# Kernel optimization log

Hardware: AMD Instinct MI355X
Metric: run time of the kernel (lower is better)

Reference implementation:

```python
import jax, jax.numpy as jnp
import numpy as np

NUM_HEADS = 8
S = 8192
D = 64          # PROJECTION_WIDTH
WORD_WIDTH = 512  # NUM_HEADS * D


def setup_inputs() -> dict:
    key = jax.random.key(0)
    kq, kk, kv, kw = jax.random.split(key, 4)
    q = jax.random.normal(kq, (S, D), dtype=jnp.float32)
    k = jax.random.normal(kk, (S, D), dtype=jnp.float32)
    v = jax.random.normal(kv, (S, D), dtype=jnp.float32)
    w_o = jax.random.normal(kw, (NUM_HEADS * D, WORD_WIDTH), dtype=jnp.float32)
    return {"q": q, "k": k, "v": v, "w_o": w_o}


def reference(q, k, v, w_o):
    # q_dot_k = q @ k.T / sqrt(d); softmax over dim=1 (rows); no mask.
    scale = 1.0 / jnp.sqrt(jnp.asarray(q.shape[1], dtype=q.dtype))
    scores = jnp.einsum('sd,td->st', q, k) * scale          # [S, S]
    attn = jax.nn.softmax(scores, axis=1)                   # [S, S]
    head = jnp.einsum('st,td->sd', attn, v)                 # [S, D]
    # All NUM_HEADS SelfAttentionLayers share the same (q,k,v) and have no
    # per-head parameters, so concatenating the heads is a tile of one head.
    concat = jnp.tile(head, (1, NUM_HEADS))                 # [S, NUM_HEADS*D]
    return concat @ w_o                                     # [S, WORD_WIDTH]
```

## Files before the change

### kernel.cpp

```cpp
#include <hip/hip_runtime.h>
#include <hip/hip_bf16.h>

typedef _Float16 half8 __attribute__((ext_vector_type(8)));
typedef __fp16 fp16x2 __attribute__((ext_vector_type(2)));
typedef __attribute__((ext_vector_type(4))) float floatx4;
typedef __attribute__((ext_vector_type(2))) float floatx2;

#define MFMAH(a, b, c) __builtin_amdgcn_mfma_f32_16x16x32_f16((a), (b), (c), 0, 0, 0)

#define SEQ 8192
#define SCALE_LOG2E 0.18033688011112042f

__device__ __forceinline__ unsigned pkh(float a, float b) {
    union { fp16x2 h; unsigned u; } cv;
    cv.h = __builtin_amdgcn_cvt_pkrtz(a, b);
    return cv.u;
}
__device__ __forceinline__ void gload16(const void* gptr, void* lptr) {
    __builtin_amdgcn_global_load_lds(
        (const __attribute__((address_space(1))) void*)gptr,
        (__attribute__((address_space(3))) void*)lptr, 16, 0, 0);
}
__device__ __forceinline__ void block_barrier() {
    asm volatile("" ::: "memory");
    __builtin_amdgcn_s_barrier();
    asm volatile("" ::: "memory");
}

__global__ __launch_bounds__(256) void prep_kernel(
        const float* __restrict__ kg, const float* __restrict__ vg,
        const float* __restrict__ w_o, _Float16* __restrict__ kf,
        _Float16* __restrict__ vt, float* __restrict__ weff) {
    const int bid = blockIdx.x, tid = threadIdx.x;
    if (bid < 256) {
        int e = (bid * 256 + tid) * 8;
        floatx4 a = *(const floatx4*)(kg + e);
        floatx4 b = *(const floatx4*)(kg + e + 4);
        half8 h;
        h[0] = (_Float16)a[0]; h[1] = (_Float16)a[1]; h[2] = (_Float16)a[2]; h[3] = (_Float16)a[3];
        h[4] = (_Float16)b[0]; h[5] = (_Float16)b[1]; h[6] = (_Float16)b[2]; h[7] = (_Float16)b[3];
        *(half8*)(kf + e) = h;
    } else if (bid < 384) {
        __shared__ _Float16 T[64][72];
        const int t0 = (bid - 256) * 64;
        {
            int r = tid >> 2, cs = (tid & 3) * 16;
            const float* vp = vg + (size_t)(t0 + r) * 64 + cs;
            half8 h0, h1;
#pragma unroll
            for (int j = 0; j < 8; ++j) { h0[j] = (_Float16)vp[j]; h1[j] = (_Float16)vp[8 + j]; }
            *(half8*)&T[r][cs] = h0;
            *(half8*)&T[r][cs + 8] = h1;
        }
        __syncthreads();
        {
            int d = tid >> 2, ts = (tid & 3) * 16;
            half8 o0, o1;
#pragma unroll
            for (int j = 0; j < 8; ++j) { o0[j] = T[ts + j][d]; o1[j] = T[ts + 8 + j][d]; }
            *(half8*)(vt + (size_t)d * SEQ + t0 + ts) = o0;
            *(half8*)(vt + (size_t)d * SEQ + t0 + ts + 8) = o1;
        }
    } else {
        int idx = (bid - 384) * 256 + tid;
        int d = idx >> 9, j = idx & 511;
        float s = 0.f;
#pragma unroll
        for (int h = 0; h < 8; ++h) s += w_o[((h * 64 + d) << 9) + j];
        weff[idx] = s;
    }
}

__global__ __launch_bounds__(256, 4) void flash_kernel(
        const float* __restrict__ qg, const _Float16* __restrict__ kf,
        const _Float16* __restrict__ vt, float* __restrict__ pacc,
        float* __restrict__ pl, int kvlen) {
    __shared__ __align__(16) char smem[32768];

    const int tid  = threadIdx.x;
    const int lane = tid & 63;
    const int w    = tid >> 6;
    const int l15  = lane & 15;
    const int kgi  = lane >> 4;
    const int qbase = blockIdx.x * 128;
    const int split = blockIdx.y;
    const int kv0   = split * kvlen;
    const int nt    = kvlen >> 6;

    const int r0 = tid >> 3;
    const int g8 = (((tid & 7) ^ (r0 & 7)) << 3);
    const int pr0 = ((r0 >> 2) & 3) * 8 + ((r0 >> 4) & 1) * 4 + (r0 & 3);

    auto STAGE = [&](int bsel, int kvb) {
        char* b = smem + bsel * 16384;
        const size_t ko = (size_t)(kvb + pr0) * 64 + g8;
        const size_t vo = (size_t)r0 * SEQ + kvb + g8;
        gload16(kf + ko,                    b + tid * 16);
        gload16(kf + ko + 32 * 64,          b + 4096  + tid * 16);
        gload16(vt + vo,                    b + 8192  + tid * 16);
        gload16(vt + vo + (size_t)32 * SEQ, b + 12288 + tid * 16);
    };

    const float* qp = qg + (size_t)(qbase + w * 32 + l15) * 64 + kgi * 8;
    floatx4 qv[2][2][2];
#pragma unroll
    for (int qf = 0; qf < 2; ++qf)
#pragma unroll
        for (int kc = 0; kc < 2; ++kc) {
            qv[qf][kc][0] = *(const floatx4*)(qp + qf * 16 * 64 + kc * 32);
            qv[qf][kc][1] = *(const floatx4*)(qp + qf * 16 * 64 + kc * 32 + 4);
        }

    STAGE(0, kv0);
    STAGE(1, kv0 + 64);

    half8 qh[2][2];
#pragma unroll
    for (int qf = 0; qf < 2; ++qf)
#pragma unroll
        for (int kc = 0; kc < 2; ++kc) {
            half8 h;
#pragma unroll
            for (int i = 0; i < 4; ++i) {
                h[i]     = (_Float16)(qv[qf][kc][0][i] * SCALE_LOG2E);
                h[i + 4] = (_Float16)(qv[qf][kc][1][i] * SCALE_LOG2E);
            }
            qh[qf][kc] = h;
        }

    floatx4 acc[2][4];
#pragma unroll
    for (int qf = 0; qf < 2; ++qf)
#pragma unroll
        for (int i = 0; i < 4; ++i) acc[qf][i] = (floatx4){0.f, 0.f, 0.f, 0.f};
    floatx4 lacc[2] = {(floatx4){0.f, 0.f, 0.f, 0.f}, (floatx4){0.f, 0.f, 0.f, 0.f}};
    const half8 vone = {(_Float16)1.f, (_Float16)1.f, (_Float16)1.f, (_Float16)1.f,
                        (_Float16)1.f, (_Float16)1.f, (_Float16)1.f, (_Float16)1.f};

    asm volatile("s_waitcnt vmcnt(4)" ::: "memory");
    block_barrier();

    for (int t = 0; t < nt; ++t) {
        const _Float16* KL = (const _Float16*)(smem + (t & 1) * 16384);
        const _Float16* VL = KL + 4096;

        floatx4 st[2][4];
#pragma unroll
        for (int qf = 0; qf < 2; ++qf)
#pragma unroll
            for (int ct = 0; ct < 4; ++ct) st[qf][ct] = (floatx4){0.f, 0.f, 0.f, 0.f};
        __builtin_amdgcn_s_setprio(1);
#pragma unroll
        for (int ct = 0; ct < 4; ++ct) {
            const int row = ct * 16 + l15;
#pragma unroll
            for (int kc = 0; kc < 2; ++kc) {
                const int go = (((kc * 4 + kgi) ^ (row & 7)) << 3);
                const half8 kh = *(const half8*)(KL + row * 64 + go);
                st[0][ct] = MFMAH(kh, qh[0][kc], st[0][ct]);
                st[1][ct] = MFMAH(kh, qh[1][kc], st[1][ct]);
            }
        }
        __builtin_amdgcn_s_setprio(0);

        half8 pbh[2][2];
#pragma unroll
        for (int qf = 0; qf < 2; ++qf) {
#pragma unroll
            for (int ct = 0; ct < 4; ++ct)
#pragma unroll
                for (int r = 0; r < 4; ++r)
                    st[qf][ct][r] = __builtin_amdgcn_exp2f(st[qf][ct][r]);
#pragma unroll
            for (int kc = 0; kc < 2; ++kc) {
                union { unsigned u[4]; half8 h; } pb;
                pb.u[0] = pkh(st[qf][2 * kc][0],     st[qf][2 * kc][1]);
                pb.u[1] = pkh(st[qf][2 * kc][2],     st[qf][2 * kc][3]);
                pb.u[2] = pkh(st[qf][2 * kc + 1][0], st[qf][2 * kc + 1][1]);
                pb.u[3] = pkh(st[qf][2 * kc + 1][2], st[qf][2 * kc + 1][3]);
                pbh[qf][kc] = pb.h;
            }
        }

        __builtin_amdgcn_s_setprio(1);
#pragma unroll
        for (int kc = 0; kc < 2; ++kc) {
            lacc[0] = MFMAH(vone, pbh[0][kc], lacc[0]);
            lacc[1] = MFMAH(vone, pbh[1][kc], lacc[1]);
#pragma unroll
            for (int db = 0; db < 4; ++db) {
                const int row = db * 16 + l15;
                const int go = (((kc * 4 + kgi) ^ (row & 7)) << 3);
                const half8 va = *(const half8*)(VL + row * 64 + go);
                acc[0][db] = MFMAH(va, pbh[0][kc], acc[0][db]);
                acc[1][db] = MFMAH(va, pbh[1][kc], acc[1][db]);
            }
        }
        __builtin_amdgcn_s_setprio(0);

        if (t + 1 < nt) {
            block_barrier();
            if (t + 2 < nt) {
                STAGE(t & 1, kv0 + (t + 2) * 64);
                asm volatile("s_waitcnt vmcnt(4)" ::: "memory");
            } else {
                asm volatile("s_waitcnt vmcnt(0)" ::: "memory");
            }
            block_barrier();
        }
    }

    block_barrier();
    float* Tw = (float*)(smem + w * 4352);
#pragma unroll
    for (int qf = 0; qf < 2; ++qf) {
#pragma unroll
        for (int db = 0; db < 4; ++db)
#pragma unroll
            for (int r = 0; r < 4; ++r)
                Tw[l15 * 68 + db * 16 + kgi * 4 + r] = acc[qf][db][r];
        {
            const int qrow = lane >> 2, gg = lane & 3;
            float* orow = pacc + ((size_t)split * SEQ + qbase + w * 32 + qf * 16 + qrow) * 64 + gg * 16;
#pragma unroll
            for (int i = 0; i < 4; ++i)
                *(floatx4*)(orow + i * 4) = *(const floatx4*)&Tw[qrow * 68 + gg * 16 + i * 4];
        }
        if (lane < 16) {
            pl[(size_t)split * SEQ + qbase + w * 32 + qf * 16 + lane] = lacc[qf][0];
        }
        __builtin_amdgcn_s_barrier();
    }
}

__global__ __launch_bounds__(256) void combineproj_kernel(
        const float* __restrict__ pacc, const float* __restrict__ pl,
        const float* __restrict__ weff, float* __restrict__ out, int KS) {
    __shared__ float hlds[16][64];
    const int tid = threadIdx.x;
    const int s0 = blockIdx.x * 16;
    {
        const int row = tid >> 4, d0 = (tid & 15) * 4;
        const int qq = s0 + row;
        floatx4 A = (floatx4){0.f, 0.f, 0.f, 0.f};
        float L = 0.f;
        for (int s2 = 0; s2 < KS; ++s2) {
            L += pl[(size_t)s2 * SEQ + qq];
            A += *(const floatx4*)&pacc[((size_t)s2 * SEQ + qq) * 64 + d0];
        }
        A *= (1.0f / L);
        *(floatx4*)&hlds[row][d0] = A;
    }
    __syncthreads();
    const int j0 = tid * 2;
    float a0[16], a1[16];
#pragma unroll
    for (int s = 0; s < 16; ++s) { a0[s] = 0.f; a1[s] = 0.f; }
    for (int d4 = 0; d4 < 16; ++d4) {
        floatx2 wv[4];
#pragma unroll
        for (int dd = 0; dd < 4; ++dd)
            wv[dd] = *(const floatx2*)&weff[(size_t)(d4 * 4 + dd) * 512 + j0];
#pragma unroll
        for (int s = 0; s < 16; ++s) {
            floatx4 h = *(const floatx4*)&hlds[s][d4 * 4];
#pragma unroll
            for (int dd = 0; dd < 4; ++dd) {
                a0[s] += h[dd] * wv[dd][0];
                a1[s] += h[dd] * wv[dd][1];
            }
        }
    }
#pragma unroll
    for (int s = 0; s < 16; ++s) {
        floatx2 o = {a0[s], a1[s]};
        *(floatx2*)&out[(size_t)(s0 + s) * 512 + j0] = o;
    }
}

extern "C" void kernel_launch(void* const* d_in, const int* in_sizes, int n_in,
                              void* d_out, int out_size, void* d_ws, size_t ws_size,
                              hipStream_t stream) {
    const float* q   = (const float*)d_in[0];
    const float* k   = (const float*)d_in[1];
    const float* v   = (const float*)d_in[2];
    const float* w_o = (const float*)d_in[3];
    float* out = (float*)d_out;

    const size_t weff_sz = 64 * 512 * sizeof(float);
    const size_t h_sz    = (size_t)SEQ * 64 * sizeof(_Float16);
    auto need = [&](int ks) {
        return weff_sz + 2 * h_sz
               + (size_t)ks * SEQ * 64 * sizeof(float)
               + (size_t)ks * SEQ * sizeof(float);
    };
    int KS = 1;
    if (ws_size >= need(8)) KS = 8;
    else if (ws_size >= need(4)) KS = 4;
    else if (ws_size >= need(2)) KS = 2;

    char* p = (char*)d_ws;
    float* weff = (float*)p;  p += weff_sz;
    float* pacc = (float*)p;  p += (size_t)KS * SEQ * 64 * sizeof(float);
    float* pl   = (float*)p;  p += (size_t)KS * SEQ * sizeof(float);
    _Float16* kf = (_Float16*)p;  p += h_sz;
    _Float16* vt = (_Float16*)p;

    prep_kernel<<<dim3(512), dim3(256), 0, stream>>>(k, v, w_o, kf, vt, weff);
    flash_kernel<<<dim3(SEQ / 128, KS), dim3(256), 0, stream>>>(q, kf, vt, pacc, pl, SEQ / KS);
    combineproj_kernel<<<dim3(SEQ / 16), dim3(256), 0, stream>>>(pacc, pl, weff, out, KS);
}
```

Baseline: 107.6 us.

## Double query rows per flash block and add a 16-way KV split

```diff
diff --git a/kernel.cpp b/kernel.cpp
--- a/kernel.cpp
+++ b/kernel.cpp
@@ -71,7 +71,7 @@
     }
 }
 
-__global__ __launch_bounds__(256, 4) void flash_kernel(
+__global__ __launch_bounds__(256, 2) void flash_kernel(
         const float* __restrict__ qg, const _Float16* __restrict__ kf,
         const _Float16* __restrict__ vt, float* __restrict__ pacc,
         float* __restrict__ pl, int kvlen) {
@@ -82,7 +82,7 @@
     const int w    = tid >> 6;
     const int l15  = lane & 15;
     const int kgi  = lane >> 4;
-    const int qbase = blockIdx.x * 128;
+    const int qbase = blockIdx.x * 256;
     const int split = blockIdx.y;
     const int kv0   = split * kvlen;
     const int nt    = kvlen >> 6;
@@ -101,10 +101,10 @@
         gload16(vt + vo + (size_t)32 * SEQ, b + 12288 + tid * 16);
     };
 
-    const float* qp = qg + (size_t)(qbase + w * 32 + l15) * 64 + kgi * 8;
-    floatx4 qv[2][2][2];
-#pragma unroll
-    for (int qf = 0; qf < 2; ++qf)
+    const float* qp = qg + (size_t)(qbase + w * 64 + l15) * 64 + kgi * 8;
+    floatx4 qv[4][2][2];
+#pragma unroll
+    for (int qf = 0; qf < 4; ++qf)
 #pragma unroll
         for (int kc = 0; kc < 2; ++kc) {
             qv[qf][kc][0] = *(const floatx4*)(qp + qf * 16 * 64 + kc * 32);
@@ -114,9 +114,9 @@
     STAGE(0, kv0);
     STAGE(1, kv0 + 64);
 
-    half8 qh[2][2];
-#pragma unroll
-    for (int qf = 0; qf < 2; ++qf)
+    half8 qh[4][2];
+#pragma unroll
+    for (int qf = 0; qf < 4; ++qf)
 #pragma unroll
         for (int kc = 0; kc < 2; ++kc) {
             half8 h;
@@ -128,12 +128,14 @@
             qh[qf][kc] = h;
         }
 
-    floatx4 acc[2][4];
-#pragma unroll
-    for (int qf = 0; qf < 2; ++qf)
+    floatx4 acc[4][4];
+#pragma unroll
+    for (int qf = 0; qf < 4; ++qf)
 #pragma unroll
         for (int i = 0; i < 4; ++i) acc[qf][i] = (floatx4){0.f, 0.f, 0.f, 0.f};
-    floatx4 lacc[2] = {(floatx4){0.f, 0.f, 0.f, 0.f}, (floatx4){0.f, 0.f, 0.f, 0.f}};
+    floatx4 lacc[4];
+#pragma unroll
+    for (int qf = 0; qf < 4; ++qf) lacc[qf] = (floatx4){0.f, 0.f, 0.f, 0.f};
     const half8 vone = {(_Float16)1.f, (_Float16)1.f, (_Float16)1.f, (_Float16)1.f,
                         (_Float16)1.f, (_Float16)1.f, (_Float16)1.f, (_Float16)1.f};
 
@@ -144,40 +146,42 @@
         const _Float16* KL = (const _Float16*)(smem + (t & 1) * 16384);
         const _Float16* VL = KL + 4096;
 
-        floatx4 st[2][4];
-#pragma unroll
-        for (int qf = 0; qf < 2; ++qf)
-#pragma unroll
-            for (int ct = 0; ct < 4; ++ct) st[qf][ct] = (floatx4){0.f, 0.f, 0.f, 0.f};
-        __builtin_amdgcn_s_setprio(1);
+        half8 khr[4][2];
 #pragma unroll
         for (int ct = 0; ct < 4; ++ct) {
             const int row = ct * 16 + l15;
 #pragma unroll
             for (int kc = 0; kc < 2; ++kc) {
                 const int go = (((kc * 4 + kgi) ^ (row & 7)) << 3);
-                const half8 kh = *(const half8*)(KL + row * 64 + go);
-                st[0][ct] = MFMAH(kh, qh[0][kc], st[0][ct]);
-                st[1][ct] = MFMAH(kh, qh[1][kc], st[1][ct]);
-            }
-        }
-        __builtin_amdgcn_s_setprio(0);
-
-        half8 pbh[2][2];
-#pragma unroll
-        for (int qf = 0; qf < 2; ++qf) {
+                khr[ct][kc] = *(const half8*)(KL + row * 64 + go);
+            }
+        }
+
+        half8 pbh[4][2];
+#pragma unroll
+        for (int qf = 0; qf < 4; ++qf) {
+            floatx4 st[4];
+#pragma unroll
+            for (int ct = 0; ct < 4; ++ct) st[ct] = (floatx4){0.f, 0.f, 0.f, 0.f};
+            __builtin_amdgcn_s_setprio(1);
 #pragma unroll
             for (int ct = 0; ct < 4; ++ct)
 #pragma unroll
+                for (int kc = 0; kc < 2; ++kc)
+                    st[ct] = MFMAH(khr[ct][kc], qh[qf][kc], st[ct]);
+            __builtin_amdgcn_s_setprio(0);
+#pragma unroll
+            for (int ct = 0; ct < 4; ++ct)
+#pragma unroll
                 for (int r = 0; r < 4; ++r)
-                    st[qf][ct][r] = __builtin_amdgcn_exp2f(st[qf][ct][r]);
+                    st[ct][r] = __builtin_amdgcn_exp2f(st[ct][r]);
 #pragma unroll
             for (int kc = 0; kc < 2; ++kc) {
                 union { unsigned u[4]; half8 h; } pb;
-                pb.u[0] = pkh(st[qf][2 * kc][0],     st[qf][2 * kc][1]);
-                pb.u[1] = pkh(st[qf][2 * kc][2],     st[qf][2 * kc][3]);
-                pb.u[2] = pkh(st[qf][2 * kc + 1][0], st[qf][2 * kc + 1][1]);
-                pb.u[3] = pkh(st[qf][2 * kc + 1][2], st[qf][2 * kc + 1][3]);
+                pb.u[0] = pkh(st[2 * kc][0],     st[2 * kc][1]);
+                pb.u[1] = pkh(st[2 * kc][2],     st[2 * kc][3]);
+                pb.u[2] = pkh(st[2 * kc + 1][0], st[2 * kc + 1][1]);
+                pb.u[3] = pkh(st[2 * kc + 1][2], st[2 * kc + 1][3]);
                 pbh[qf][kc] = pb.h;
             }
         }
@@ -185,15 +189,17 @@
         __builtin_amdgcn_s_setprio(1);
 #pragma unroll
         for (int kc = 0; kc < 2; ++kc) {
-            lacc[0] = MFMAH(vone, pbh[0][kc], lacc[0]);
-            lacc[1] = MFMAH(vone, pbh[1][kc], lacc[1]);
+#pragma unroll
+            for (int qf = 0; qf < 4; ++qf)
+                lacc[qf] = MFMAH(vone, pbh[qf][kc], lacc[qf]);
 #pragma unroll
             for (int db = 0; db < 4; ++db) {
                 const int row = db * 16 + l15;
                 const int go = (((kc * 4 + kgi) ^ (row & 7)) << 3);
                 const half8 va = *(const half8*)(VL + row * 64 + go);
-                acc[0][db] = MFMAH(va, pbh[0][kc], acc[0][db]);
-                acc[1][db] = MFMAH(va, pbh[1][kc], acc[1][db]);
+#pragma unroll
+                for (int qf = 0; qf < 4; ++qf)
+                    acc[qf][db] = MFMAH(va, pbh[qf][kc], acc[qf][db]);
             }
         }
         __builtin_amdgcn_s_setprio(0);
@@ -213,7 +219,7 @@
     block_barrier();
     float* Tw = (float*)(smem + w * 4352);
 #pragma unroll
-    for (int qf = 0; qf < 2; ++qf) {
+    for (int qf = 0; qf < 4; ++qf) {
 #pragma unroll
         for (int db = 0; db < 4; ++db)
 #pragma unroll
@@ -221,13 +227,13 @@
                 Tw[l15 * 68 + db * 16 + kgi * 4 + r] = acc[qf][db][r];
         {
             const int qrow = lane >> 2, gg = lane & 3;
-            float* orow = pacc + ((size_t)split * SEQ + qbase + w * 32 + qf * 16 + qrow) * 64 + gg * 16;
+            float* orow = pacc + ((size_t)split * SEQ + qbase + w * 64 + qf * 16 + qrow) * 64 + gg * 16;
 #pragma unroll
             for (int i = 0; i < 4; ++i)
                 *(floatx4*)(orow + i * 4) = *(const floatx4*)&Tw[qrow * 68 + gg * 16 + i * 4];
         }
         if (lane < 16) {
-            pl[(size_t)split * SEQ + qbase + w * 32 + qf * 16 + lane] = lacc[qf][0];
+            pl[(size_t)split * SEQ + qbase + w * 64 + qf * 16 + lane] = lacc[qf][0];
         }
         __builtin_amdgcn_s_barrier();
     }
@@ -295,7 +301,8 @@
                + (size_t)ks * SEQ * sizeof(float);
     };
     int KS = 1;
-    if (ws_size >= need(8)) KS = 8;
+    if (ws_size >= need(16)) KS = 16;
+    else if (ws_size >= need(8)) KS = 8;
     else if (ws_size >= need(4)) KS = 4;
     else if (ws_size >= need(2)) KS = 2;
 
@@ -307,6 +314,6 @@
     _Float16* vt = (_Float16*)p;
 
     prep_kernel<<<dim3(512), dim3(256), 0, stream>>>(k, v, w_o, kf, vt, weff);
-    flash_kernel<<<dim3(SEQ / 128, KS), dim3(256), 0, stream>>>(q, kf, vt, pacc, pl, SEQ / KS);
+    flash_kernel<<<dim3(SEQ / 256, KS), dim3(256), 0, stream>>>(q, kf, vt, pacc, pl, SEQ / KS);
     combineproj_kernel<<<dim3(SEQ / 16), dim3(256), 0, stream>>>(pacc, pl, weff, out, KS);
 }
```

Result: slower. 112.2 us (+4.2%).
